# Optimization experiments

Measured on AMD Instinct MI355X. Metric: run time of the kernel, lower is better.

## Reference

```python
import jax, jax.numpy as jnp
import numpy as np

H = 16
N_TASKS, N_DATA, N_DEV = 400_000, 200_000, 8


def _edges(key, n_src, n_dst, e):
    k1, k2 = jax.random.split(key)
    src = jax.random.randint(k1, (e,), 0, n_src)
    dst = jax.random.randint(k2, (e,), 0, n_dst)
    return jnp.stack([src, dst]).astype(jnp.int64)


def setup_inputs() -> dict:
    key = jax.random.key(0)
    ks = jax.random.split(key, 16)
    inp = {
        "x_tasks": jax.random.normal(ks[0], (N_TASKS, 12), jnp.float32),
        "x_data": jax.random.normal(ks[1], (N_DATA, 5), jnp.float32),
        "x_devices": jax.random.normal(ks[2], (N_DEV, 12), jnp.float32),
        "ei_data_tasks": _edges(ks[3], N_DATA, N_TASKS, 1_600_000),
        "ei_tasks_data": _edges(ks[4], N_TASKS, N_DATA, 1_600_000),
        "ei_tasks_devices": _edges(ks[5], N_TASKS, N_DEV, 400_000),
        "ei_devices_tasks": _edges(ks[6], N_DEV, N_TASKS, 400_000),
        "ei_data_devices": _edges(ks[7], N_DATA, N_DEV, 200_000),
        "ei_devices_data": _edges(ks[8], N_DEV, N_DATA, 200_000),
        "ei_tt_to": _edges(ks[9], N_TASKS, N_TASKS, 800_000),
        "ei_tt_from": _edges(ks[10], N_TASKS, N_TASKS, 800_000),
        # stacked GraphConv weights, grouped by input dim
        # W_rel5:  [0]=data->tasks, [1]=data->devices
        "W_rel5": jax.random.normal(ks[11], (2, 5, H), jnp.float32) * 0.3,
        # W_rel12: [0]=tasks->data,[1]=tasks->devices,[2]=devices->tasks,[3]=devices->data,[4]=tt_to,[5]=tt_from
        "W_rel12": jax.random.normal(ks[12], (6, 12, H), jnp.float32) * 0.2,
        # b_rel order: dt_t, t_d, t_dev, dev_t, d_dev, dev_d, tt_to, tt_from
        "b_rel": jax.random.normal(ks[13], (8, H), jnp.float32) * 0.1,
        # W_root5: [0]=tasks->data (dst data), [1]=devices->data
        "W_root5": jax.random.normal(ks[14], (2, 5, H), jnp.float32) * 0.3,
        # W_root12: [0]=data->tasks,[1]=tasks->devices,[2]=devices->tasks,[3]=data->devices,[4]=tt_to,[5]=tt_from
        "W_root12": jax.random.normal(ks[15], (6, 12, H), jnp.float32) * 0.2,
        # LayerNorm params: [0]=tasks, [1]=data, [2]=devices
        "ln_gamma": jnp.ones((3, H), jnp.float32),
        "ln_beta": jnp.zeros((3, H), jnp.float32),
    }
    return inp


def _graph_conv(x_src, x_dst, ei, W_rel, b_rel, W_root):
    # PyG GraphConv(aggr='add'): lin_rel(scatter_add(x_src[src] -> dst)) + lin_root(x_dst)
    agg = jax.ops.segment_sum(x_src[ei[0]], ei[1], num_segments=x_dst.shape[0])
    return agg @ W_rel + b_rel + x_dst @ W_root


def _layer_norm(x, gamma, beta, eps=1e-5):
    mu = jnp.mean(x, axis=-1, keepdims=True)
    var = jnp.mean(jnp.square(x - mu), axis=-1, keepdims=True)
    return (x - mu) * jax.lax.rsqrt(var + eps) * gamma + beta


def reference(x_tasks, x_data, x_devices,
              ei_data_tasks, ei_tasks_data, ei_tasks_devices, ei_devices_tasks,
              ei_data_devices, ei_devices_data, ei_tt_to, ei_tt_from,
              W_rel5, W_rel12, b_rel, W_root5, W_root12, ln_gamma, ln_beta):
    # HeteroConv(aggr='sum'): sum relation outputs per destination node type
    tasks = (
        _graph_conv(x_data, x_tasks, ei_data_tasks, W_rel5[0], b_rel[0], W_root12[0])
        + _graph_conv(x_devices, x_tasks, ei_devices_tasks, W_rel12[2], b_rel[3], W_root12[2])
        + _graph_conv(x_tasks, x_tasks, ei_tt_to, W_rel12[4], b_rel[6], W_root12[4])
        + _graph_conv(x_tasks, x_tasks, ei_tt_from, W_rel12[5], b_rel[7], W_root12[5])
    )
    data = (
        _graph_conv(x_tasks, x_data, ei_tasks_data, W_rel12[0], b_rel[1], W_root5[0])
        + _graph_conv(x_devices, x_data, ei_devices_data, W_rel12[3], b_rel[5], W_root5[1])
    )
    devices = (
        _graph_conv(x_tasks, x_devices, ei_tasks_devices, W_rel12[1], b_rel[2], W_root12[1])
        + _graph_conv(x_data, x_devices, ei_data_devices, W_rel5[1], b_rel[4], W_root12[3])
    )
    slope = 0.01
    tasks = jax.nn.leaky_relu(_layer_norm(tasks, ln_gamma[0], ln_beta[0]), slope)
    data = jax.nn.leaky_relu(_layer_norm(data, ln_gamma[1], ln_beta[1]), slope)
    devices = jax.nn.leaky_relu(_layer_norm(devices, ln_gamma[2], ln_beta[2]), slope)
    return tasks, data, devices
```

## Files before the change

kernel.cpp:

```cpp
#include <hip/hip_runtime.h>
#include <hip/hip_fp16.h>

#define LRELU(v) ((v) >= 0.0f ? (v) : 0.01f * (v))
#define EPB 8192
#define SHIFT_T 7
#define SHIFT_D 8
#define MAXB 3200

struct PartDesc {
    const int* src; const int* dst;
    unsigned int* part; int* cursor;
    int E, B, cap, shift, chunk0;
};

struct PrepArgs {
    PartDesc r[6];
    int part_end;
    const int *tdev_e; int E_tdev; int sd12_b0, sd12_nb;
    const int *ddev_e; int E_ddev; int sd5_b0, sd5_nb;
    const float *x_tasks, *x_data, *x_dev;
    float *aggT_dev, *aggD_dev;
    __half *h_tasks; int NT; int ct_b0;
    __half *h_data;  int ND; int cd_b0;
};

template<int F>
__device__ __forceinline__ void loadrow(const float* __restrict__ x, unsigned s, float* v) {
    const float* p = x + (size_t)s * F;
    #pragma unroll
    for (int f = 0; f < F; ++f) v[f] = p[f];
}
template<>
__device__ __forceinline__ void loadrow<12>(const float* __restrict__ x, unsigned s, float* v) {
    const float4* p = (const float4*)(x + (size_t)s * 12);
    float4 a = p[0], b = p[1], c = p[2];
    v[0]=a.x; v[1]=a.y; v[2]=a.z; v[3]=a.w;
    v[4]=b.x; v[5]=b.y; v[6]=b.z; v[7]=b.w;
    v[8]=c.x; v[9]=c.y; v[10]=c.z; v[11]=c.w;
}

template<int F>
__device__ void scatter_dev_body(const float* __restrict__ x, const int* __restrict__ src,
                                 const int* __restrict__ dst, int E,
                                 float* __restrict__ agg, float* s_agg,
                                 int bl, int nb, int t)
{
    for (int i = t; i < 8 * F; i += 256) s_agg[i] = 0.0f;
    __syncthreads();
    const int stride = nb * 256;
    for (int e = bl * 256 + t; e < E; e += stride) {
        float v[F];
        loadrow<F>(x, (unsigned)src[e], v);
        int d = dst[e];
        #pragma unroll
        for (int f = 0; f < F; ++f) atomicAdd(&s_agg[d * F + f], v[f]);
    }
    __syncthreads();
    if (t < 8 * F) atomicAdd(&agg[t], s_agg[t]);
}

__global__ __launch_bounds__(256)
void prep_k(PrepArgs A)
{
    __shared__ int shmem[2 * MAXB];
    const int bid = blockIdx.x;
    const int t = threadIdx.x;

    if (bid < A.part_end) {
        int* hist = shmem;
        int* base = shmem + MAXB;
        int ri = 0;
        #pragma unroll
        for (int k = 1; k < 6; ++k) if (bid >= A.r[k].chunk0) ri = k;
        const PartDesc d = A.r[ri];
        const int e0 = (bid - d.chunk0) * EPB;
        const int e1 = min(d.E, e0 + EPB);
        const int B = d.B, sh = d.shift;
        const unsigned mask = (1u << sh) - 1u;

        for (int i = t; i < B; i += 256) hist[i] = 0;
        __syncthreads();
        for (int e = e0 + t; e < e1; e += 256)
            atomicAdd(&hist[d.dst[e] >> sh], 1);
        __syncthreads();
        for (int i = t; i < B; i += 256) {
            int h = hist[i];
            base[i] = h ? atomicAdd(&d.cursor[i], h) : 0;
            hist[i] = 0;
        }
        __syncthreads();
        for (int e = e0 + t; e < e1; e += 256) {
            int dd = d.dst[e];
            int b = dd >> sh;
            int r = atomicAdd(&hist[b], 1) + base[b];
            if (r < d.cap)
                d.part[(size_t)b * d.cap + r] =
                    ((unsigned)d.src[e] << sh) | ((unsigned)dd & mask);
        }
    } else if (bid < A.sd5_b0) {
        scatter_dev_body<12>(A.x_tasks, A.tdev_e, A.tdev_e + A.E_tdev, A.E_tdev,
                             A.aggT_dev, (float*)shmem, bid - A.sd12_b0, A.sd12_nb, t);
    } else if (bid < A.ct_b0) {
        scatter_dev_body<5>(A.x_data, A.ddev_e, A.ddev_e + A.E_ddev, A.E_ddev,
                            A.aggD_dev, (float*)shmem, bid - A.sd5_b0, A.sd5_nb, t);
    } else if (bid < A.cd_b0) {
        int row = (bid - A.ct_b0) * 256 + t;
        if (row < A.NT) {
            const float* xr = A.x_tasks + (size_t)row * 12;
            __half h[16];
            #pragma unroll
            for (int j = 0; j < 12; ++j) h[j] = __float2half(xr[j]);
            #pragma unroll
            for (int j = 12; j < 16; ++j) h[j] = __half(0.0f);
            uint4* dst = (uint4*)(A.h_tasks + (size_t)row * 16);
            dst[0] = *(const uint4*)h;
            dst[1] = *(const uint4*)(h + 8);
        }
    } else {
        int row = (bid - A.cd_b0) * 256 + t;
        if (row < A.ND) {
            const float* xr = A.x_data + (size_t)row * 5;
            __half h[8];
            #pragma unroll
            for (int j = 0; j < 5; ++j) h[j] = __float2half(xr[j]);
            #pragma unroll
            for (int j = 5; j < 8; ++j) h[j] = __half(0.0f);
            *(uint4*)(A.h_data + (size_t)row * 8) = *(const uint4*)h;
        }
    }
}

struct LoadH8 {
    const __half* x;
    __device__ __forceinline__ void operator()(unsigned s, float* v) const {
        uint4 u = *(const uint4*)(x + (size_t)s * 8);
        const __half2* h = (const __half2*)&u;
        float2 f0 = __half22float2(h[0]);
        float2 f1 = __half22float2(h[1]);
        float2 f2 = __half22float2(h[2]);
        v[0] = f0.x; v[1] = f0.y; v[2] = f1.x; v[3] = f1.y; v[4] = f2.x;
    }
};
struct LoadH16 {
    const __half* x;
    __device__ __forceinline__ void operator()(unsigned s, float* v) const {
        const uint4* p = (const uint4*)(x + (size_t)s * 16);
        uint4 u0 = p[0], u1 = p[1];
        const __half2* a = (const __half2*)&u0;
        const __half2* b = (const __half2*)&u1;
        float2 f;
        f = __half22float2(a[0]); v[0] = f.x; v[1] = f.y;
        f = __half22float2(a[1]); v[2] = f.x; v[3] = f.y;
        f = __half22float2(a[2]); v[4] = f.x; v[5] = f.y;
        f = __half22float2(a[3]); v[6] = f.x; v[7] = f.y;
        f = __half22float2(b[0]); v[8] = f.x; v[9] = f.y;
        f = __half22float2(b[1]); v[10] = f.x; v[11] = f.y;
    }
};
struct LoadF12 {
    const float* x;
    __device__ __forceinline__ void operator()(unsigned s, float* v) const {
        loadrow<12>(x, s, v);
    }
};

template<int F>
__device__ __forceinline__ void addrow(float* a, const float* v) {
    #pragma unroll
    for (int f = 0; f < F; ++f) atomicAdd(a + f, v[f]);
}

template<int F, int STRIDE, int BASE, int SHIFT, class LD>
__device__ __forceinline__
void agg_rel4(const unsigned* __restrict__ p, int cnt, LD ld, float* acc, int t)
{
    constexpr unsigned MASK = (1u << SHIFT) - 1u;
    int i = 4 * t;
    for (; i + 3 < cnt; i += 1024) {
        uint4 e = *(const uint4*)(p + i);
        float v0[F], v1[F], v2[F], v3[F];
        ld(e.x >> SHIFT, v0);
        ld(e.y >> SHIFT, v1);
        ld(e.z >> SHIFT, v2);
        ld(e.w >> SHIFT, v3);
        addrow<F>(acc + (e.x & MASK) * STRIDE + BASE, v0);
        addrow<F>(acc + (e.y & MASK) * STRIDE + BASE, v1);
        addrow<F>(acc + (e.z & MASK) * STRIDE + BASE, v2);
        addrow<F>(acc + (e.w & MASK) * STRIDE + BASE, v3);
    }
    const int jend = min(i + 4, cnt);
    for (int j = i; j < jend; ++j) {
        unsigned e = p[j];
        float v[F];
        ld(e >> SHIFT, v);
        addrow<F>(acc + (e & MASK) * STRIDE + BASE, v);
    }
}

template<int NF>
__device__ __forceinline__
void dot_ln_store(const float* __restrict__ f, const float* __restrict__ sW,
                  const float* __restrict__ sb, const float* __restrict__ sg,
                  const float* __restrict__ sbt, float* __restrict__ op)
{
    float o[16];
    #pragma unroll
    for (int k = 0; k < 16; ++k) o[k] = sb[k];
    const float4* w4 = (const float4*)sW;
    #pragma unroll
    for (int j = 0; j < NF; ++j) {
        const float fj = f[j];
        float4 w0 = w4[j*4+0], w1 = w4[j*4+1], w2 = w4[j*4+2], w3 = w4[j*4+3];
        o[0] =fmaf(fj,w0.x,o[0]);  o[1] =fmaf(fj,w0.y,o[1]);
        o[2] =fmaf(fj,w0.z,o[2]);  o[3] =fmaf(fj,w0.w,o[3]);
        o[4] =fmaf(fj,w1.x,o[4]);  o[5] =fmaf(fj,w1.y,o[5]);
        o[6] =fmaf(fj,w1.z,o[6]);  o[7] =fmaf(fj,w1.w,o[7]);
        o[8] =fmaf(fj,w2.x,o[8]);  o[9] =fmaf(fj,w2.y,o[9]);
        o[10]=fmaf(fj,w2.z,o[10]); o[11]=fmaf(fj,w2.w,o[11]);
        o[12]=fmaf(fj,w3.x,o[12]); o[13]=fmaf(fj,w3.y,o[13]);
        o[14]=fmaf(fj,w3.z,o[14]); o[15]=fmaf(fj,w3.w,o[15]);
    }
    float mu = 0.0f;
    #pragma unroll
    for (int k = 0; k < 16; ++k) mu += o[k];
    mu *= 0.0625f;
    float var = 0.0f;
    #pragma unroll
    for (int k = 0; k < 16; ++k) { float d = o[k] - mu; var = fmaf(d, d, var); }
    var *= 0.0625f;
    const float r = rsqrtf(var + 1e-5f);
    #pragma unroll
    for (int k = 0; k < 16; ++k) {
        float v = (o[k] - mu) * r * sg[k] + sbt[k];
        op[k] = LRELU(v);
    }
}

struct FinArgs {
    const unsigned *p_dt, *p_devt, *p_to, *p_from, *p_td, *p_devd;
    const int *c_dt, *c_devt, *c_to, *c_from, *c_td, *c_devd;
    int cap_dt, cap_devt, cap_to, cap_from, cap_td, cap_devd;
    const float *x_tasks, *x_data, *x_dev;
    const __half *h_tasks, *h_data;
    const float *W_rel5, *W_rel12, *b_rel, *W_root5, *W_root12, *ln_g, *ln_b;
    float *out_tasks, *out_data;
    int NT, ND, Bt;
};

__global__ __launch_bounds__(256, 4)
void agg_finalize_k(FinArgs A)
{
    __shared__ __align__(16) float lds[6912];
    const int t = threadIdx.x;

    if ((int)blockIdx.x < A.Bt) {
        float* sW  = lds;
        float* sb  = lds + 848;
        float* sg  = lds + 864;
        float* sbt = lds + 880;
        float* acc = lds + 896;
        const int b  = blockIdx.x;
        const int n0 = b << SHIFT_T;
        const int nn = min(128, A.NT - n0);
        for (int i = t; i < 80; i += 256) sW[i] = A.W_rel5[i];
        for (int i = t; i < 192; i += 256) {
            sW[80  + i] = A.W_rel12[384 + i];
            sW[272 + i] = A.W_rel12[768 + i];
            sW[464 + i] = A.W_rel12[960 + i];
            sW[656 + i] = A.W_root12[i] + A.W_root12[384 + i]
                        + A.W_root12[768 + i] + A.W_root12[960 + i];
        }
        if (t < 16) {
            sb[t]  = A.b_rel[t] + A.b_rel[48 + t] + A.b_rel[96 + t] + A.b_rel[112 + t];
            sg[t]  = A.ln_g[t];
            sbt[t] = A.ln_b[t];
        }
        for (int i = t; i < 128 * 41; i += 256) acc[i] = 0.0f;
        __syncthreads();

        agg_rel4<5, 41, 0, SHIFT_T>(A.p_dt   + (size_t)b * A.cap_dt,   min(A.c_dt[b],   A.cap_dt),   LoadH8{A.h_data},   acc, t);
        agg_rel4<12,41, 5, SHIFT_T>(A.p_devt + (size_t)b * A.cap_devt, min(A.c_devt[b], A.cap_devt), LoadF12{A.x_dev},   acc, t);
        agg_rel4<12,41,17, SHIFT_T>(A.p_to   + (size_t)b * A.cap_to,   min(A.c_to[b],   A.cap_to),   LoadH16{A.h_tasks}, acc, t);
        agg_rel4<12,41,29, SHIFT_T>(A.p_from + (size_t)b * A.cap_from, min(A.c_from[b], A.cap_from), LoadH16{A.h_tasks}, acc, t);
        __syncthreads();

        if (t < nn) {
            float f[53];
            #pragma unroll
            for (int j = 0; j < 41; ++j) f[j] = acc[t * 41 + j];
            const float* xr = A.x_tasks + (size_t)(n0 + t) * 12;
            #pragma unroll
            for (int j = 0; j < 12; ++j) f[41 + j] = xr[j];
            dot_ln_store<53>(f, sW, sb, sg, sbt, A.out_tasks + (size_t)(n0 + t) * 16);
        }
    } else {
        float* sW  = lds;
        float* sb  = lds + 464;
        float* sg  = lds + 480;
        float* sbt = lds + 496;
        float* acc = lds + 512;
        const int b  = blockIdx.x - A.Bt;
        const int n0 = b << SHIFT_D;
        const int nn = min(256, A.ND - n0);
        for (int i = t; i < 192; i += 256) {
            sW[i]       = A.W_rel12[i];
            sW[192 + i] = A.W_rel12[576 + i];
        }
        for (int i = t; i < 80; i += 256)
            sW[384 + i] = A.W_root5[i] + A.W_root5[80 + i];
        if (t < 16) {
            sb[t]  = A.b_rel[16 + t] + A.b_rel[80 + t];
            sg[t]  = A.ln_g[16 + t];
            sbt[t] = A.ln_b[16 + t];
        }
        for (int i = t; i < 256 * 25; i += 256) acc[i] = 0.0f;
        __syncthreads();

        agg_rel4<12,25, 0, SHIFT_D>(A.p_td   + (size_t)b * A.cap_td,   min(A.c_td[b],   A.cap_td),   LoadH16{A.h_tasks}, acc, t);
        agg_rel4<12,25,12, SHIFT_D>(A.p_devd + (size_t)b * A.cap_devd, min(A.c_devd[b], A.cap_devd), LoadF12{A.x_dev},   acc, t);
        __syncthreads();

        if (t < nn) {
            float f[29];
            #pragma unroll
            for (int j = 0; j < 24; ++j) f[j] = acc[t * 25 + j];
            const float* xr = A.x_data + (size_t)(n0 + t) * 5;
            #pragma unroll
            for (int j = 0; j < 5; ++j) f[24 + j] = xr[j];
            dot_ln_store<29>(f, sW, sb, sg, sbt, A.out_data + (size_t)(n0 + t) * 16);
        }
    }
}

__global__ void finalize_dev_k(const float* __restrict__ aggT, const float* __restrict__ aggD,
                               const float* __restrict__ x,
                               const float* __restrict__ W_rel12, const float* __restrict__ W_rel5,
                               const float* __restrict__ b_rel, const float* __restrict__ W_root12,
                               const float* __restrict__ ln_g, const float* __restrict__ ln_b,
                               float* __restrict__ out, int N)
{
    int i = threadIdx.x;
    if (i >= N) return;
    float acc[16];
    #pragma unroll
    for (int k = 0; k < 16; ++k) acc[k] = b_rel[32 + k] + b_rel[64 + k];
    #pragma unroll
    for (int j = 0; j < 12; ++j) {
        float fj = aggT[i * 12 + j];
        #pragma unroll
        for (int k = 0; k < 16; ++k) acc[k] = fmaf(fj, W_rel12[192 + j * 16 + k], acc[k]);
    }
    #pragma unroll
    for (int j = 0; j < 5; ++j) {
        float fj = aggD[i * 5 + j];
        #pragma unroll
        for (int k = 0; k < 16; ++k) acc[k] = fmaf(fj, W_rel5[80 + j * 16 + k], acc[k]);
    }
    #pragma unroll
    for (int j = 0; j < 12; ++j) {
        float fj = x[i * 12 + j];
        #pragma unroll
        for (int k = 0; k < 16; ++k)
            acc[k] = fmaf(fj, W_root12[192 + j * 16 + k] + W_root12[576 + j * 16 + k], acc[k]);
    }
    float mu = 0.0f;
    #pragma unroll
    for (int k = 0; k < 16; ++k) mu += acc[k];
    mu *= 0.0625f;
    float var = 0.0f;
    #pragma unroll
    for (int k = 0; k < 16; ++k) { float d = acc[k] - mu; var = fmaf(d, d, var); }
    var *= 0.0625f;
    const float r = rsqrtf(var + 1e-5f);
    #pragma unroll
    for (int k = 0; k < 16; ++k) {
        float v = (acc[k] - mu) * r * ln_g[32 + k] + ln_b[32 + k];
        out[i * 16 + k] = LRELU(v);
    }
}

extern "C" void kernel_launch(void* const* d_in, const int* in_sizes, int n_in,
                              void* d_out, int out_size, void* d_ws, size_t ws_size,
                              hipStream_t stream)
{
    const float* x_tasks = (const float*)d_in[0];
    const float* x_data  = (const float*)d_in[1];
    const float* x_dev   = (const float*)d_in[2];
    const int* ei_dt    = (const int*)d_in[3];
    const int* ei_td    = (const int*)d_in[4];
    const int* ei_tdev  = (const int*)d_in[5];
    const int* ei_devt  = (const int*)d_in[6];
    const int* ei_ddev  = (const int*)d_in[7];
    const int* ei_devd  = (const int*)d_in[8];
    const int* ei_to    = (const int*)d_in[9];
    const int* ei_from  = (const int*)d_in[10];
    const float* W_rel5   = (const float*)d_in[11];
    const float* W_rel12  = (const float*)d_in[12];
    const float* b_rel    = (const float*)d_in[13];
    const float* W_root5  = (const float*)d_in[14];
    const float* W_root12 = (const float*)d_in[15];
    const float* ln_g     = (const float*)d_in[16];
    const float* ln_b     = (const float*)d_in[17];

    const int NT   = in_sizes[0] / 12;
    const int ND   = in_sizes[1] / 5;
    const int NDEV = in_sizes[2] / 12;
    const int E_dt   = in_sizes[3]  / 2;
    const int E_td   = in_sizes[4]  / 2;
    const int E_tdev = in_sizes[5]  / 2;
    const int E_devt = in_sizes[6]  / 2;
    const int E_ddev = in_sizes[7]  / 2;
    const int E_devd = in_sizes[8]  / 2;
    const int E_to   = in_sizes[9]  / 2;
    const int E_from = in_sizes[10] / 2;

    const int B_t = (NT + 127) / 128;
    const int B_d = (ND + 255) / 256;

    auto capf = [](int E, int B) {
        int mean = E / B + 1;
        int c = mean + 256 + mean / 8;
        return (c + 3) & ~3;
    };
    const int cap_dt   = capf(E_dt,   B_t);
    const int cap_devt = capf(E_devt, B_t);
    const int cap_to   = capf(E_to,   B_t);
    const int cap_from = capf(E_from, B_t);
    const int cap_td   = capf(E_td,   B_d);
    const int cap_devd = capf(E_devd, B_d);

    float* ws = (float*)d_ws;
    size_t o = 0;
    int* c_dt   = (int*)(ws + o); o += MAXB;
    int* c_devt = (int*)(ws + o); o += MAXB;
    int* c_to   = (int*)(ws + o); o += MAXB;
    int* c_from = (int*)(ws + o); o += MAXB;
    int* c_td   = (int*)(ws + o); o += 800;
    int* c_devd = (int*)(ws + o); o += 800;
    float* aggT_dev = ws + o; o += 96;
    float* aggD_dev = ws + o; o += 48;
    const size_t zero_bytes = o * sizeof(float);
    o = (o + 3) & ~(size_t)3;
    __half* h_tasks = (__half*)(ws + o); o += (size_t)NT * 8;
    __half* h_data  = (__half*)(ws + o); o += (size_t)ND * 4;
    unsigned* p_dt   = (unsigned*)(ws + o); o += (size_t)B_t * cap_dt;
    unsigned* p_devt = (unsigned*)(ws + o); o += (size_t)B_t * cap_devt;
    unsigned* p_to   = (unsigned*)(ws + o); o += (size_t)B_t * cap_to;
    unsigned* p_from = (unsigned*)(ws + o); o += (size_t)B_t * cap_from;
    unsigned* p_td   = (unsigned*)(ws + o); o += (size_t)B_d * cap_td;
    unsigned* p_devd = (unsigned*)(ws + o); o += (size_t)B_d * cap_devd;

    hipMemsetAsync(d_ws, 0, zero_bytes, stream);

    auto nc = [](int e) { return (e + EPB - 1) / EPB; };
    PrepArgs pa;
    int ch = 0;
    pa.r[0] = { ei_dt,   ei_dt   + E_dt,   p_dt,   c_dt,   E_dt,   B_t, cap_dt,   SHIFT_T, ch }; ch += nc(E_dt);
    pa.r[1] = { ei_devt, ei_devt + E_devt, p_devt, c_devt, E_devt, B_t, cap_devt, SHIFT_T, ch }; ch += nc(E_devt);
    pa.r[2] = { ei_to,   ei_to   + E_to,   p_to,   c_to,   E_to,   B_t, cap_to,   SHIFT_T, ch }; ch += nc(E_to);
    pa.r[3] = { ei_from, ei_from + E_from, p_from, c_from, E_from, B_t, cap_from, SHIFT_T, ch }; ch += nc(E_from);
    pa.r[4] = { ei_td,   ei_td   + E_td,   p_td,   c_td,   E_td,   B_d, cap_td,   SHIFT_D, ch }; ch += nc(E_td);
    pa.r[5] = { ei_devd, ei_devd + E_devd, p_devd, c_devd, E_devd, B_d, cap_devd, SHIFT_D, ch }; ch += nc(E_devd);
    pa.part_end = ch;
    pa.tdev_e = ei_tdev; pa.E_tdev = E_tdev; pa.sd12_b0 = ch; pa.sd12_nb = 192; ch += 192;
    pa.ddev_e = ei_ddev; pa.E_ddev = E_ddev; pa.sd5_b0  = ch; pa.sd5_nb  = 96;  ch += 96;
    pa.x_tasks = x_tasks; pa.x_data = x_data; pa.x_dev = x_dev;
    pa.aggT_dev = aggT_dev; pa.aggD_dev = aggD_dev;
    pa.h_tasks = h_tasks; pa.NT = NT; pa.ct_b0 = ch; ch += (NT + 255) / 256;
    pa.h_data  = h_data;  pa.ND = ND; pa.cd_b0 = ch; ch += (ND + 255) / 256;

    prep_k<<<ch, 256, 0, stream>>>(pa);

    float* out_tasks = (float*)d_out;
    float* out_data  = out_tasks + (size_t)NT * 16;
    float* out_dev   = out_data  + (size_t)ND * 16;

    FinArgs fa;
    fa.p_dt = p_dt; fa.p_devt = p_devt; fa.p_to = p_to; fa.p_from = p_from;
    fa.p_td = p_td; fa.p_devd = p_devd;
    fa.c_dt = c_dt; fa.c_devt = c_devt; fa.c_to = c_to; fa.c_from = c_from;
    fa.c_td = c_td; fa.c_devd = c_devd;
    fa.cap_dt = cap_dt; fa.cap_devt = cap_devt; fa.cap_to = cap_to;
    fa.cap_from = cap_from; fa.cap_td = cap_td; fa.cap_devd = cap_devd;
    fa.x_tasks = x_tasks; fa.x_data = x_data; fa.x_dev = x_dev;
    fa.h_tasks = h_tasks; fa.h_data = h_data;
    fa.W_rel5 = W_rel5; fa.W_rel12 = W_rel12; fa.b_rel = b_rel;
    fa.W_root5 = W_root5; fa.W_root12 = W_root12; fa.ln_g = ln_g; fa.ln_b = ln_b;
    fa.out_tasks = out_tasks; fa.out_data = out_data;
    fa.NT = NT; fa.ND = ND; fa.Bt = B_t;

    agg_finalize_k<<<B_t + B_d, 256, 0, stream>>>(fa);

    finalize_dev_k<<<1, 64, 0, stream>>>(
        aggT_dev, aggD_dev, x_dev,
        W_rel12, W_rel5, b_rel, W_root12, ln_g, ln_b, out_dev, NDEV);
}
```

Before: 637.4 us.

## Split per-relation aggregation into separate kernel with fp16 intermediates

```diff
diff --git a/kernel.cpp b/kernel.cpp
--- a/kernel.cpp
+++ b/kernel.cpp
@@ -3,14 +3,13 @@
 
 #define LRELU(v) ((v) >= 0.0f ? (v) : 0.01f * (v))
 #define EPB 8192
-#define SHIFT_T 7
-#define SHIFT_D 8
-#define MAXB 3200
+#define SHIFT 7
+#define PAIRS 1600
 
 struct PartDesc {
     const int* src; const int* dst;
-    unsigned int* part; int* cursor;
-    int E, B, cap, shift, chunk0;
+    unsigned* part; int* cursor;
+    int E, B, cap, chunk0;
 };
 
 struct PrepArgs {
@@ -62,47 +61,53 @@
 __global__ __launch_bounds__(256)
 void prep_k(PrepArgs A)
 {
-    __shared__ int shmem[2 * MAXB];
+    __shared__ unsigned shp[2 * PAIRS];
     const int bid = blockIdx.x;
     const int t = threadIdx.x;
 
     if (bid < A.part_end) {
-        int* hist = shmem;
-        int* base = shmem + MAXB;
+        unsigned* hist = shp;
+        unsigned* base = shp + PAIRS;
         int ri = 0;
         #pragma unroll
         for (int k = 1; k < 6; ++k) if (bid >= A.r[k].chunk0) ri = k;
         const PartDesc d = A.r[ri];
         const int e0 = (bid - d.chunk0) * EPB;
         const int e1 = min(d.E, e0 + EPB);
-        const int B = d.B, sh = d.shift;
-        const unsigned mask = (1u << sh) - 1u;
-
-        for (int i = t; i < B; i += 256) hist[i] = 0;
+        const int npair = (d.B + 1) >> 1;
+
+        for (int i = t; i < npair; i += 256) hist[i] = 0u;
         __syncthreads();
-        for (int e = e0 + t; e < e1; e += 256)
-            atomicAdd(&hist[d.dst[e] >> sh], 1);
+        for (int e = e0 + t; e < e1; e += 256) {
+            int b = d.dst[e] >> SHIFT;
+            atomicAdd(&hist[b >> 1], 1u << ((b & 1) << 4));
+        }
         __syncthreads();
-        for (int i = t; i < B; i += 256) {
-            int h = hist[i];
-            base[i] = h ? atomicAdd(&d.cursor[i], h) : 0;
-            hist[i] = 0;
+        for (int i = t; i < npair; i += 256) {
+            unsigned h = hist[i];
+            unsigned lo = h & 0xffffu, hi = h >> 16;
+            unsigned blo = lo ? (unsigned)atomicAdd(&d.cursor[2 * i],     (int)lo) : 0u;
+            unsigned bhi = hi ? (unsigned)atomicAdd(&d.cursor[2 * i + 1], (int)hi) : 0u;
+            base[i] = (blo & 0xffffu) | (bhi << 16);
+            hist[i] = 0u;
         }
         __syncthreads();
         for (int e = e0 + t; e < e1; e += 256) {
             int dd = d.dst[e];
-            int b = dd >> sh;
-            int r = atomicAdd(&hist[b], 1) + base[b];
-            if (r < d.cap)
-                d.part[(size_t)b * d.cap + r] =
-                    ((unsigned)d.src[e] << sh) | ((unsigned)dd & mask);
+            int b = dd >> SHIFT;
+            unsigned s16 = (unsigned)(b & 1) << 4;
+            unsigned r = atomicAdd(&hist[b >> 1], 1u << s16);
+            unsigned idx = ((r >> s16) & 0xffffu) + ((base[b >> 1] >> s16) & 0xffffu);
+            if ((int)idx < d.cap)
+                d.part[(size_t)b * d.cap + idx] =
+                    ((unsigned)d.src[e] << SHIFT) | ((unsigned)dd & 127u);
         }
     } else if (bid < A.sd5_b0) {
         scatter_dev_body<12>(A.x_tasks, A.tdev_e, A.tdev_e + A.E_tdev, A.E_tdev,
-                             A.aggT_dev, (float*)shmem, bid - A.sd12_b0, A.sd12_nb, t);
+                             A.aggT_dev, (float*)shp, bid - A.sd12_b0, A.sd12_nb, t);
     } else if (bid < A.ct_b0) {
         scatter_dev_body<5>(A.x_data, A.ddev_e, A.ddev_e + A.E_ddev, A.E_ddev,
-                            A.aggD_dev, (float*)shmem, bid - A.sd5_b0, A.sd5_nb, t);
+                            A.aggD_dev, (float*)shp, bid - A.sd5_b0, A.sd5_nb, t);
     } else if (bid < A.cd_b0) {
         int row = (bid - A.ct_b0) * 256 + t;
         if (row < A.NT) {
@@ -170,11 +175,10 @@
     for (int f = 0; f < F; ++f) atomicAdd(a + f, v[f]);
 }
 
-template<int F, int STRIDE, int BASE, int SHIFT, class LD>
+template<int F, class LD>
 __device__ __forceinline__
 void agg_rel4(const unsigned* __restrict__ p, int cnt, LD ld, float* acc, int t)
 {
-    constexpr unsigned MASK = (1u << SHIFT) - 1u;
     int i = 4 * t;
     for (; i + 3 < cnt; i += 1024) {
         uint4 e = *(const uint4*)(p + i);
@@ -183,18 +187,82 @@
         ld(e.y >> SHIFT, v1);
         ld(e.z >> SHIFT, v2);
         ld(e.w >> SHIFT, v3);
-        addrow<F>(acc + (e.x & MASK) * STRIDE + BASE, v0);
-        addrow<F>(acc + (e.y & MASK) * STRIDE + BASE, v1);
-        addrow<F>(acc + (e.z & MASK) * STRIDE + BASE, v2);
-        addrow<F>(acc + (e.w & MASK) * STRIDE + BASE, v3);
+        addrow<F>(acc + (e.x & 127u) * F, v0);
+        addrow<F>(acc + (e.y & 127u) * F, v1);
+        addrow<F>(acc + (e.z & 127u) * F, v2);
+        addrow<F>(acc + (e.w & 127u) * F, v3);
     }
     const int jend = min(i + 4, cnt);
     for (int j = i; j < jend; ++j) {
         unsigned e = p[j];
         float v[F];
         ld(e >> SHIFT, v);
-        addrow<F>(acc + (e & MASK) * STRIDE + BASE, v);
-    }
+        addrow<F>(acc + (e & 127u) * F, v);
+    }
+}
+
+struct AggDesc { const unsigned* part; const int* cursor; int cap, b0; };
+struct AggArgs {
+    AggDesc r[6];
+    const __half *h_tasks, *h_data; const float* x_dev;
+    __half *aD_t, *aDev_t, *aTo, *aFrom, *aT_d, *aDev_d;
+    int NT, ND;
+};
+
+template<int F, int OSTR, class LD>
+__device__ __forceinline__
+void agg_body(const unsigned* p, int cnt, LD ld, float* acc,
+              __half* out, int N, int n0, int t)
+{
+    const int nn = min(128, N - n0);
+    for (int i = t; i < 128 * F; i += 256) acc[i] = 0.0f;
+    __syncthreads();
+    agg_rel4<F>(p, cnt, ld, acc, t);
+    __syncthreads();
+    __half* o = out + (size_t)n0 * OSTR;
+    for (int i = t; i < nn * OSTR; i += 256) {
+        int n = i / OSTR, c = i - n * OSTR;
+        float v = (c < F) ? acc[n * F + c] : 0.0f;
+        o[i] = __float2half(v);
+    }
+}
+
+__global__ __launch_bounds__(256, 6)
+void agg_k(AggArgs A)
+{
+    __shared__ float acc[128 * 12];
+    const int bid = blockIdx.x;
+    const int t = threadIdx.x;
+    int ri = 0;
+    #pragma unroll
+    for (int k = 1; k < 6; ++k) if (bid >= A.r[k].b0) ri = k;
+    const AggDesc d = A.r[ri];
+    const int b = bid - d.b0;
+    const unsigned* p = d.part + (size_t)b * d.cap;
+    const int cnt = min(d.cursor[b], d.cap);
+    const int n0 = b << SHIFT;
+
+    if (ri == 0)      agg_body<5, 6 >(p, cnt, LoadH8 {A.h_data},  acc, A.aD_t,   A.NT, n0, t);
+    else if (ri == 1) agg_body<12, 12>(p, cnt, LoadF12{A.x_dev},   acc, A.aDev_t, A.NT, n0, t);
+    else if (ri == 2) agg_body<12, 12>(p, cnt, LoadH16{A.h_tasks}, acc, A.aTo,    A.NT, n0, t);
+    else if (ri == 3) agg_body<12, 12>(p, cnt, LoadH16{A.h_tasks}, acc, A.aFrom,  A.NT, n0, t);
+    else if (ri == 4) agg_body<12, 12>(p, cnt, LoadH16{A.h_tasks}, acc, A.aT_d,   A.ND, n0, t);
+    else              agg_body<12, 12>(p, cnt, LoadF12{A.x_dev},   acc, A.aDev_d, A.ND, n0, t);
+}
+
+__device__ __forceinline__ float2 upk(unsigned u) {
+    __half2 h = *(__half2*)&u; return __half22float2(h);
+}
+__device__ __forceinline__ void load12h(const __half* base, size_t i, float* f) {
+    const uint2* q = (const uint2*)(base + i * 12);
+    uint2 u0 = q[0], u1 = q[1], u2 = q[2];
+    float2 x;
+    x = upk(u0.x); f[0]  = x.x; f[1]  = x.y;
+    x = upk(u0.y); f[2]  = x.x; f[3]  = x.y;
+    x = upk(u1.x); f[4]  = x.x; f[5]  = x.y;
+    x = upk(u1.y); f[6]  = x.x; f[7]  = x.y;
+    x = upk(u2.x); f[8]  = x.x; f[9]  = x.y;
+    x = upk(u2.y); f[10] = x.x; f[11] = x.y;
 }
 
 template<int NF>
@@ -237,31 +305,23 @@
 }
 
 struct FinArgs {
-    const unsigned *p_dt, *p_devt, *p_to, *p_from, *p_td, *p_devd;
-    const int *c_dt, *c_devt, *c_to, *c_from, *c_td, *c_devd;
-    int cap_dt, cap_devt, cap_to, cap_from, cap_td, cap_devd;
+    const __half *aD_t, *aDev_t, *aTo, *aFrom, *aT_d, *aDev_d;
     const float *x_tasks, *x_data, *x_dev;
-    const __half *h_tasks, *h_data;
+    const float *aggT_dev, *aggD_dev;
     const float *W_rel5, *W_rel12, *b_rel, *W_root5, *W_root12, *ln_g, *ln_b;
-    float *out_tasks, *out_data;
-    int NT, ND, Bt;
+    float *out_tasks, *out_data, *out_dev;
+    int NT, ND, NDEV, Bt, Bd;
 };
 
 __global__ __launch_bounds__(256, 4)
-void agg_finalize_k(FinArgs A)
-{
-    __shared__ __align__(16) float lds[6912];
+void finalize_k(FinArgs A)
+{
+    __shared__ __align__(16) float lds[896];
+    const int bid = blockIdx.x;
     const int t = threadIdx.x;
 
-    if ((int)blockIdx.x < A.Bt) {
-        float* sW  = lds;
-        float* sb  = lds + 848;
-        float* sg  = lds + 864;
-        float* sbt = lds + 880;
-        float* acc = lds + 896;
-        const int b  = blockIdx.x;
-        const int n0 = b << SHIFT_T;
-        const int nn = min(128, A.NT - n0);
+    if (bid < A.Bt) {
+        float* sW = lds; float* sb = lds + 848; float* sg = lds + 864; float* sbt = lds + 880;
         for (int i = t; i < 80; i += 256) sW[i] = A.W_rel5[i];
         for (int i = t; i < 192; i += 256) {
             sW[80  + i] = A.W_rel12[384 + i];
@@ -275,33 +335,28 @@
             sg[t]  = A.ln_g[t];
             sbt[t] = A.ln_b[t];
         }
-        for (int i = t; i < 128 * 41; i += 256) acc[i] = 0.0f;
         __syncthreads();
-
-        agg_rel4<5, 41, 0, SHIFT_T>(A.p_dt   + (size_t)b * A.cap_dt,   min(A.c_dt[b],   A.cap_dt),   LoadH8{A.h_data},   acc, t);
-        agg_rel4<12,41, 5, SHIFT_T>(A.p_devt + (size_t)b * A.cap_devt, min(A.c_devt[b], A.cap_devt), LoadF12{A.x_dev},   acc, t);
-        agg_rel4<12,41,17, SHIFT_T>(A.p_to   + (size_t)b * A.cap_to,   min(A.c_to[b],   A.cap_to),   LoadH16{A.h_tasks}, acc, t);
-        agg_rel4<12,41,29, SHIFT_T>(A.p_from + (size_t)b * A.cap_from, min(A.c_from[b], A.cap_from), LoadH16{A.h_tasks}, acc, t);
-        __syncthreads();
-
-        if (t < nn) {
+        const int i = bid * 256 + t;
+        if (i < A.NT) {
             float f[53];
-            #pragma unroll
-            for (int j = 0; j < 41; ++j) f[j] = acc[t * 41 + j];
-            const float* xr = A.x_tasks + (size_t)(n0 + t) * 12;
-            #pragma unroll
-            for (int j = 0; j < 12; ++j) f[41 + j] = xr[j];
-            dot_ln_store<53>(f, sW, sb, sg, sbt, A.out_tasks + (size_t)(n0 + t) * 16);
-        }
-    } else {
-        float* sW  = lds;
-        float* sb  = lds + 464;
-        float* sg  = lds + 480;
-        float* sbt = lds + 496;
-        float* acc = lds + 512;
-        const int b  = blockIdx.x - A.Bt;
-        const int n0 = b << SHIFT_D;
-        const int nn = min(256, A.ND - n0);
+            {
+                const unsigned* q = (const unsigned*)A.aD_t + (size_t)i * 3;
+                unsigned u0 = q[0], u1 = q[1], u2 = q[2];
+                float2 a = upk(u0), b = upk(u1), c = upk(u2);
+                f[0] = a.x; f[1] = a.y; f[2] = b.x; f[3] = b.y; f[4] = c.x;
+            }
+            load12h(A.aDev_t, i, f + 5);
+            load12h(A.aTo,   i, f + 17);
+            load12h(A.aFrom, i, f + 29);
+            const float4* xr = (const float4*)(A.x_tasks + (size_t)i * 12);
+            float4 x0 = xr[0], x1 = xr[1], x2 = xr[2];
+            f[41]=x0.x; f[42]=x0.y; f[43]=x0.z; f[44]=x0.w;
+            f[45]=x1.x; f[46]=x1.y; f[47]=x1.z; f[48]=x1.w;
+            f[49]=x2.x; f[50]=x2.y; f[51]=x2.z; f[52]=x2.w;
+            dot_ln_store<53>(f, sW, sb, sg, sbt, A.out_tasks + (size_t)i * 16);
+        }
+    } else if (bid < A.Bt + A.Bd) {
+        float* sW = lds; float* sb = lds + 464; float* sg = lds + 480; float* sbt = lds + 496;
         for (int i = t; i < 192; i += 256) {
             sW[i]       = A.W_rel12[i];
             sW[192 + i] = A.W_rel12[576 + i];
@@ -313,69 +368,57 @@
             sg[t]  = A.ln_g[16 + t];
             sbt[t] = A.ln_b[16 + t];
         }
-        for (int i = t; i < 256 * 25; i += 256) acc[i] = 0.0f;
         __syncthreads();
-
-        agg_rel4<12,25, 0, SHIFT_D>(A.p_td   + (size_t)b * A.cap_td,   min(A.c_td[b],   A.cap_td),   LoadH16{A.h_tasks}, acc, t);
-        agg_rel4<12,25,12, SHIFT_D>(A.p_devd + (size_t)b * A.cap_devd, min(A.c_devd[b], A.cap_devd), LoadF12{A.x_dev},   acc, t);
-        __syncthreads();
-
-        if (t < nn) {
+        const int i = (bid - A.Bt) * 256 + t;
+        if (i < A.ND) {
             float f[29];
-            #pragma unroll
-            for (int j = 0; j < 24; ++j) f[j] = acc[t * 25 + j];
-            const float* xr = A.x_data + (size_t)(n0 + t) * 5;
+            load12h(A.aT_d,   i, f);
+            load12h(A.aDev_d, i, f + 12);
+            const float* xr = A.x_data + (size_t)i * 5;
             #pragma unroll
             for (int j = 0; j < 5; ++j) f[24 + j] = xr[j];
-            dot_ln_store<29>(f, sW, sb, sg, sbt, A.out_data + (size_t)(n0 + t) * 16);
-        }
-    }
-}
-
-__global__ void finalize_dev_k(const float* __restrict__ aggT, const float* __restrict__ aggD,
-                               const float* __restrict__ x,
-                               const float* __restrict__ W_rel12, const float* __restrict__ W_rel5,
-                               const float* __restrict__ b_rel, const float* __restrict__ W_root12,
-                               const float* __restrict__ ln_g, const float* __restrict__ ln_b,
-                               float* __restrict__ out, int N)
-{
-    int i = threadIdx.x;
-    if (i >= N) return;
-    float acc[16];
-    #pragma unroll
-    for (int k = 0; k < 16; ++k) acc[k] = b_rel[32 + k] + b_rel[64 + k];
-    #pragma unroll
-    for (int j = 0; j < 12; ++j) {
-        float fj = aggT[i * 12 + j];
-        #pragma unroll
-        for (int k = 0; k < 16; ++k) acc[k] = fmaf(fj, W_rel12[192 + j * 16 + k], acc[k]);
-    }
-    #pragma unroll
-    for (int j = 0; j < 5; ++j) {
-        float fj = aggD[i * 5 + j];
-        #pragma unroll
-        for (int k = 0; k < 16; ++k) acc[k] = fmaf(fj, W_rel5[80 + j * 16 + k], acc[k]);
-    }
-    #pragma unroll
-    for (int j = 0; j < 12; ++j) {
-        float fj = x[i * 12 + j];
-        #pragma unroll
-        for (int k = 0; k < 16; ++k)
-            acc[k] = fmaf(fj, W_root12[192 + j * 16 + k] + W_root12[576 + j * 16 + k], acc[k]);
-    }
-    float mu = 0.0f;
-    #pragma unroll
-    for (int k = 0; k < 16; ++k) mu += acc[k];
-    mu *= 0.0625f;
-    float var = 0.0f;
-    #pragma unroll
-    for (int k = 0; k < 16; ++k) { float d = acc[k] - mu; var = fmaf(d, d, var); }
-    var *= 0.0625f;
-    const float r = rsqrtf(var + 1e-5f);
-    #pragma unroll
-    for (int k = 0; k < 16; ++k) {
-        float v = (acc[k] - mu) * r * ln_g[32 + k] + ln_b[32 + k];
-        out[i * 16 + k] = LRELU(v);
+            dot_ln_store<29>(f, sW, sb, sg, sbt, A.out_data + (size_t)i * 16);
+        }
+    } else {
+        const int i = t;
+        if (i < A.NDEV) {
+            float acc[16];
+            #pragma unroll
+            for (int k = 0; k < 16; ++k) acc[k] = A.b_rel[32 + k] + A.b_rel[64 + k];
+            #pragma unroll
+            for (int j = 0; j < 12; ++j) {
+                float fj = A.aggT_dev[i * 12 + j];
+                #pragma unroll
+                for (int k = 0; k < 16; ++k) acc[k] = fmaf(fj, A.W_rel12[192 + j * 16 + k], acc[k]);
+            }
+            #pragma unroll
+            for (int j = 0; j < 5; ++j) {
+                float fj = A.aggD_dev[i * 5 + j];
+                #pragma unroll
+                for (int k = 0; k < 16; ++k) acc[k] = fmaf(fj, A.W_rel5[80 + j * 16 + k], acc[k]);
+            }
+            #pragma unroll
+            for (int j = 0; j < 12; ++j) {
+                float fj = A.x_dev[i * 12 + j];
+                #pragma unroll
+                for (int k = 0; k < 16; ++k)
+                    acc[k] = fmaf(fj, A.W_root12[192 + j * 16 + k] + A.W_root12[576 + j * 16 + k], acc[k]);
+            }
+            float mu = 0.0f;
+            #pragma unroll
+            for (int k = 0; k < 16; ++k) mu += acc[k];
+            mu *= 0.0625f;
+            float var = 0.0f;
+            #pragma unroll
+            for (int k = 0; k < 16; ++k) { float d = acc[k] - mu; var = fmaf(d, d, var); }
+            var *= 0.0625f;
+            const float r = rsqrtf(var + 1e-5f);
+            #pragma unroll
+            for (int k = 0; k < 16; ++k) {
+                float v = (acc[k] - mu) * r * A.ln_g[32 + k] + A.ln_b[32 + k];
+                A.out_dev[i * 16 + k] = LRELU(v);
+            }
+        }
     }
 }
 
@@ -415,11 +458,11 @@
     const int E_from = in_sizes[10] / 2;
 
     const int B_t = (NT + 127) / 128;
-    const int B_d = (ND + 255) / 256;
+    const int B_d = (ND + 127) / 128;
 
     auto capf = [](int E, int B) {
         int mean = E / B + 1;
-        int c = mean + 256 + mean / 8;
+        int c = mean + mean / 4 + 128;
         return (c + 3) & ~3;
     };
     const int cap_dt   = capf(E_dt,   B_t);
@@ -431,18 +474,24 @@
 
     float* ws = (float*)d_ws;
     size_t o = 0;
-    int* c_dt   = (int*)(ws + o); o += MAXB;
-    int* c_devt = (int*)(ws + o); o += MAXB;
-    int* c_to   = (int*)(ws + o); o += MAXB;
-    int* c_from = (int*)(ws + o); o += MAXB;
-    int* c_td   = (int*)(ws + o); o += 800;
-    int* c_devd = (int*)(ws + o); o += 800;
+    int* c_dt   = (int*)(ws + o); o += 3200;
+    int* c_devt = (int*)(ws + o); o += 3200;
+    int* c_to   = (int*)(ws + o); o += 3200;
+    int* c_from = (int*)(ws + o); o += 3200;
+    int* c_td   = (int*)(ws + o); o += 1600;
+    int* c_devd = (int*)(ws + o); o += 1600;
     float* aggT_dev = ws + o; o += 96;
     float* aggD_dev = ws + o; o += 48;
     const size_t zero_bytes = o * sizeof(float);
     o = (o + 3) & ~(size_t)3;
     __half* h_tasks = (__half*)(ws + o); o += (size_t)NT * 8;
     __half* h_data  = (__half*)(ws + o); o += (size_t)ND * 4;
+    __half* aD_t    = (__half*)(ws + o); o += (size_t)NT * 3;
+    __half* aDev_t  = (__half*)(ws + o); o += (size_t)NT * 6;
+    __half* aTo     = (__half*)(ws + o); o += (size_t)NT * 6;
+    __half* aFrom   = (__half*)(ws + o); o += (size_t)NT * 6;
+    __half* aT_d    = (__half*)(ws + o); o += (size_t)ND * 6;
+    __half* aDev_d  = (__half*)(ws + o); o += (size_t)ND * 6;
     unsigned* p_dt   = (unsigned*)(ws + o); o += (size_t)B_t * cap_dt;
     unsigned* p_devt = (unsigned*)(ws + o); o += (size_t)B_t * cap_devt;
     unsigned* p_to   = (unsigned*)(ws + o); o += (size_t)B_t * cap_to;
@@ -455,12 +504,12 @@
     auto nc = [](int e) { return (e + EPB - 1) / EPB; };
     PrepArgs pa;
     int ch = 0;
-    pa.r[0] = { ei_dt,   ei_dt   + E_dt,   p_dt,   c_dt,   E_dt,   B_t, cap_dt,   SHIFT_T, ch }; ch += nc(E_dt);
-    pa.r[1] = { ei_devt, ei_devt + E_devt, p_devt, c_devt, E_devt, B_t, cap_devt, SHIFT_T, ch }; ch += nc(E_devt);
-    pa.r[2] = { ei_to,   ei_to   + E_to,   p_to,   c_to,   E_to,   B_t, cap_to,   SHIFT_T, ch }; ch += nc(E_to);
-    pa.r[3] = { ei_from, ei_from + E_from, p_from, c_from, E_from, B_t, cap_from, SHIFT_T, ch }; ch += nc(E_from);
-    pa.r[4] = { ei_td,   ei_td   + E_td,   p_td,   c_td,   E_td,   B_d, cap_td,   SHIFT_D, ch }; ch += nc(E_td);
-    pa.r[5] = { ei_devd, ei_devd + E_devd, p_devd, c_devd, E_devd, B_d, cap_devd, SHIFT_D, ch }; ch += nc(E_devd);
+    pa.r[0] = { ei_dt,   ei_dt   + E_dt,   p_dt,   c_dt,   E_dt,   B_t, cap_dt,   ch }; ch += nc(E_dt);
+    pa.r[1] = { ei_devt, ei_devt + E_devt, p_devt, c_devt, E_devt, B_t, cap_devt, ch }; ch += nc(E_devt);
+    pa.r[2] = { ei_to,   ei_to   + E_to,   p_to,   c_to,   E_to,   B_t, cap_to,   ch }; ch += nc(E_to);
+    pa.r[3] = { ei_from, ei_from + E_from, p_from, c_from, E_from, B_t, cap_from, ch }; ch += nc(E_from);
+    pa.r[4] = { ei_td,   ei_td   + E_td,   p_td,   c_td,   E_td,   B_d, cap_td,   ch }; ch += nc(E_td);
+    pa.r[5] = { ei_devd, ei_devd + E_devd, p_devd, c_devd, E_devd, B_d, cap_devd, ch }; ch += nc(E_devd);
     pa.part_end = ch;
     pa.tdev_e = ei_tdev; pa.E_tdev = E_tdev; pa.sd12_b0 = ch; pa.sd12_nb = 192; ch += 192;
     pa.ddev_e = ei_ddev; pa.E_ddev = E_ddev; pa.sd5_b0  = ch; pa.sd5_nb  = 96;  ch += 96;
@@ -471,27 +520,35 @@
 
     prep_k<<<ch, 256, 0, stream>>>(pa);
 
+    AggArgs aa;
+    int ab = 0;
+    aa.r[0] = { p_dt,   c_dt,   cap_dt,   ab }; ab += B_t;
+    aa.r[1] = { p_devt, c_devt, cap_devt, ab }; ab += B_t;
+    aa.r[2] = { p_to,   c_to,   cap_to,   ab }; ab += B_t;
+    aa.r[3] = { p_from, c_from, cap_from, ab }; ab += B_t;
+    aa.r[4] = { p_td,   c_td,   cap_td,   ab }; ab += B_d;
+    aa.r[5] = { p_devd, c_devd, cap_devd, ab }; ab += B_d;
+    aa.h_tasks = h_tasks; aa.h_data = h_data; aa.x_dev = x_dev;
+    aa.aD_t = aD_t; aa.aDev_t = aDev_t; aa.aTo = aTo; aa.aFrom = aFrom;
+    aa.aT_d = aT_d; aa.aDev_d = aDev_d;
+    aa.NT = NT; aa.ND = ND;
+
+    agg_k<<<ab, 256, 0, stream>>>(aa);
+
     float* out_tasks = (float*)d_out;
     float* out_data  = out_tasks + (size_t)NT * 16;
     float* out_dev   = out_data  + (size_t)ND * 16;
 
     FinArgs fa;
-    fa.p_dt = p_dt; fa.p_devt = p_devt; fa.p_to = p_to; fa.p_from = p_from;
-    fa.p_td = p_td; fa.p_devd = p_devd;
-    fa.c_dt = c_dt; fa.c_devt = c_devt; fa.c_to = c_to; fa.c_from = c_from;
-    fa.c_td = c_td; fa.c_devd = c_devd;
-    fa.cap_dt = cap_dt; fa.cap_devt = cap_devt; fa.cap_to = cap_to;
-    fa.cap_from = cap_from; fa.cap_td = cap_td; fa.cap_devd = cap_devd;
+    fa.aD_t = aD_t; fa.aDev_t = aDev_t; fa.aTo = aTo; fa.aFrom = aFrom;
+    fa.aT_d = aT_d; fa.aDev_d = aDev_d;
     fa.x_tasks = x_tasks; fa.x_data = x_data; fa.x_dev = x_dev;
-    fa.h_tasks = h_tasks; fa.h_data = h_data;
+    fa.aggT_dev = aggT_dev; fa.aggD_dev = aggD_dev;
     fa.W_rel5 = W_rel5; fa.W_rel12 = W_rel12; fa.b_rel = b_rel;
     fa.W_root5 = W_root5; fa.W_root12 = W_root12; fa.ln_g = ln_g; fa.ln_b = ln_b;
-    fa.out_tasks = out_tasks; fa.out_data = out_data;
-    fa.NT = NT; fa.ND = ND; fa.Bt = B_t;
-
-    agg_finalize_k<<<B_t + B_d, 256, 0, stream>>>(fa);
-
-    finalize_dev_k<<<1, 64, 0, stream>>>(
-        aggT_dev, aggD_dev, x_dev,
-        W_rel12, W_rel5, b_rel, W_root12, ln_g, ln_b, out_dev, NDEV);
-}
+    fa.out_tasks = out_tasks; fa.out_data = out_data; fa.out_dev = out_dev;
+    fa.NT = NT; fa.ND = ND; fa.NDEV = NDEV;
+    fa.Bt = (NT + 255) / 256; fa.Bd = (ND + 255) / 256;
+
+    finalize_k<<<fa.Bt + fa.Bd + 1, 256, 0, stream>>>(fa);
+}
```

New measurement: 632.5 us. No clear change (-0.8%).
